# Kernel optimization log

Measured on AMD Instinct MI355X. Metric: run time of the kernel, lower is better.

## Reference

```python
import jax, jax.numpy as jnp
import numpy as np

EPS = 1e-8  # F.cosine_similarity default eps


def setup_inputs() -> dict:
    key = jax.random.key(0)
    k1, k2, k3, k4 = jax.random.split(key, 4)
    N, M, D, BERT_DIM = 8192, 8192, 128, 768
    return {
        "vision_feature": jax.random.normal(k1, (N, D), dtype=jnp.float32),
        "text_pooled": jax.random.normal(k2, (M, BERT_DIM), dtype=jnp.float32),
        "proj_w": jax.random.normal(k3, (D, BERT_DIM), dtype=jnp.float32) * 0.02,
        "proj_b": jax.random.normal(k4, (D,), dtype=jnp.float32) * 0.02,
    }


def reference(vision_feature, text_pooled, proj_w, proj_b):
    # proj(text_pooled): [M, 768] @ [768, D] + [D] -> [M, D]
    text_feature = text_pooled @ proj_w.T + proj_b
    # Fused cosine similarity: L2-normalize rows (with eps clamp as in
    # F.cosine_similarity), then a single [N,D]x[D,M] GEMM instead of the
    # broadcasted O(N*M*D) intermediate.
    v_norm = jnp.maximum(jnp.linalg.norm(vision_feature, axis=1, keepdims=True), EPS)
    t_norm = jnp.maximum(jnp.linalg.norm(text_feature, axis=1, keepdims=True), EPS)
    vn = vision_feature / v_norm  # [N, D]
    tn = text_feature / t_norm    # [M, D]
    similarity = vn @ tn.T        # [N, M]
    return similarity
```

## Files before the change

kernel.cpp:

```cpp
#include <hip/hip_runtime.h>
#include <stdint.h>

#define NV 8192
#define MT 8192
#define DD 128
#define KB 768

typedef __attribute__((ext_vector_type(8))) short short8;
typedef __attribute__((ext_vector_type(4))) float f32x4;

__device__ __forceinline__ ushort f2bf(float f) {
  uint32_t u = __float_as_uint(f);
  u += 0x7FFF + ((u >> 16) & 1);
  return (ushort)(u >> 16);
}

__global__ __launch_bounds__(256) void k_visnorm(const float* __restrict__ vis,
                                                 ushort* __restrict__ vn) {
  const int tx = threadIdx.x & 15;
  const int r  = blockIdx.x * 16 + (threadIdx.x >> 4);
  const float* p = vis + (size_t)r * DD + tx * 8;
  float4 a = *(const float4*)p;
  float4 b = *(const float4*)(p + 4);
  float s = a.x*a.x + a.y*a.y + a.z*a.z + a.w*a.w
          + b.x*b.x + b.y*b.y + b.z*b.z + b.w*b.w;
  s += __shfl_xor(s, 1, 16);
  s += __shfl_xor(s, 2, 16);
  s += __shfl_xor(s, 4, 16);
  s += __shfl_xor(s, 8, 16);
  const float inv = 1.0f / fmaxf(sqrtf(s), 1e-8f);
  union { ushort u[8]; uint4 v; } o;
  o.u[0] = f2bf(a.x * inv); o.u[1] = f2bf(a.y * inv);
  o.u[2] = f2bf(a.z * inv); o.u[3] = f2bf(a.w * inv);
  o.u[4] = f2bf(b.x * inv); o.u[5] = f2bf(b.y * inv);
  o.u[6] = f2bf(b.z * inv); o.u[7] = f2bf(b.w * inv);
  *(uint4*)(vn + (size_t)r * DD + tx * 8) = o.v;
}

__global__ __launch_bounds__(256) void k_cvt(const float* __restrict__ src,
                                             ushort* __restrict__ dst) {
  const size_t i = ((size_t)blockIdx.x * 256 + threadIdx.x) * 8;
  float4 a = *(const float4*)(src + i);
  float4 b = *(const float4*)(src + i + 4);
  union { ushort u[8]; uint4 v; } o;
  o.u[0] = f2bf(a.x); o.u[1] = f2bf(a.y); o.u[2] = f2bf(a.z); o.u[3] = f2bf(a.w);
  o.u[4] = f2bf(b.x); o.u[5] = f2bf(b.y); o.u[6] = f2bf(b.z); o.u[7] = f2bf(b.w);
  *(uint4*)(dst + i) = o.v;
}

__global__ __launch_bounds__(64) void k_projnorm(const ushort* __restrict__ tb,
                                                 const ushort* __restrict__ wb,
                                                 const float* __restrict__ bias,
                                                 ushort* __restrict__ tn) {
  const int lane = threadIdx.x;
  const int row0 = blockIdx.x * 16;
  const int lrow = lane & 15;
  const int g    = lane >> 4;
  const int koff = g * 8;

  const ushort* ap = tb + (size_t)(row0 + lrow) * KB + koff;
  const ushort* bp = wb + (size_t)lrow * KB + koff;

  f32x4 acc[8] = {};

#pragma unroll 4
  for (int ks = 0; ks < KB / 32; ++ks) {
    short8 a = *(const short8*)(ap + ks * 32);
#pragma unroll
    for (int n = 0; n < 8; ++n) {
      short8 b = *(const short8*)(bp + (size_t)n * 16 * KB + ks * 32);
      acc[n] = __builtin_amdgcn_mfma_f32_16x16x32_bf16(a, b, acc[n], 0, 0, 0);
    }
  }

#pragma unroll
  for (int n = 0; n < 8; ++n) {
    float bv = bias[n * 16 + lrow];
#pragma unroll
    for (int j = 0; j < 4; ++j) acc[n][j] += bv;
  }
  float s0 = 0.f, s1 = 0.f, s2 = 0.f, s3 = 0.f;
#pragma unroll
  for (int n = 0; n < 8; ++n) {
    s0 += acc[n][0] * acc[n][0];
    s1 += acc[n][1] * acc[n][1];
    s2 += acc[n][2] * acc[n][2];
    s3 += acc[n][3] * acc[n][3];
  }
#pragma unroll
  for (int d = 1; d < 16; d <<= 1) {
    s0 += __shfl_xor(s0, d, 16);
    s1 += __shfl_xor(s1, d, 16);
    s2 += __shfl_xor(s2, d, 16);
    s3 += __shfl_xor(s3, d, 16);
  }
  float inv[4];
  inv[0] = 1.0f / fmaxf(sqrtf(s0), 1e-8f);
  inv[1] = 1.0f / fmaxf(sqrtf(s1), 1e-8f);
  inv[2] = 1.0f / fmaxf(sqrtf(s2), 1e-8f);
  inv[3] = 1.0f / fmaxf(sqrtf(s3), 1e-8f);

#pragma unroll
  for (int n = 0; n < 8; ++n)
#pragma unroll
    for (int j = 0; j < 4; ++j)
      tn[(size_t)(row0 + g * 4 + j) * DD + n * 16 + lrow] = f2bf(acc[n][j] * inv[j]);
}

__global__ __launch_bounds__(256, 2) void k_sim(const ushort* __restrict__ vn,
                                                const ushort* __restrict__ tn,
                                                float* __restrict__ out) {
  __shared__ ushort ls[32768];
  ushort* lsA = ls;
  ushort* lsB = ls + 16384;
  float*  lsf = (float*)ls;

  const int lin  = blockIdx.x;
  const int nlin = (lin & 7) * 512 + (lin >> 3);
  const int by   = nlin >> 6;
  const int bx   = nlin & 63;
  const int row0 = by * 128;
  const int col0 = bx * 128;

  const int t    = threadIdx.x;
  const int lane = t & 63;
  const int wave = t >> 6;

#pragma unroll
  for (int i = 0; i < 8; ++i) {
    const int fi  = i * 256 + t;
    const int row = fi >> 4;
    uint4 va = *(const uint4*)(vn + (size_t)row0 * DD + fi * 8);
    uint4 vb = *(const uint4*)(tn + (size_t)col0 * DD + fi * 8);
    const int idx = (fi * 8) ^ ((row & 7) << 3);
    *(uint4*)(lsA + idx) = va;
    *(uint4*)(lsB + idx) = vb;
  }
  __syncthreads();

  const int wr = wave >> 1;
  const int wc = wave & 1;
  const int lrow = lane & 15;
  const int kgrp = lane >> 4;

  f32x4 acc[4][4] = {};

#pragma unroll
  for (int ks = 0; ks < 4; ++ks) {
    short8 a[4], b[4];
#pragma unroll
    for (int m = 0; m < 4; ++m) {
      const int r = wr * 64 + m * 16 + lrow;
      const int c = ks * 32 + kgrp * 8;
      a[m] = *(const short8*)(lsA + ((r * 128 + c) ^ ((r & 7) << 3)));
    }
#pragma unroll
    for (int n = 0; n < 4; ++n) {
      const int r = wc * 64 + n * 16 + lrow;
      const int c = ks * 32 + kgrp * 8;
      b[n] = *(const short8*)(lsB + ((r * 128 + c) ^ ((r & 7) << 3)));
    }
#pragma unroll
    for (int m = 0; m < 4; ++m)
#pragma unroll
      for (int n = 0; n < 4; ++n)
        acc[m][n] = __builtin_amdgcn_mfma_f32_16x16x32_bf16(a[m], b[n], acc[m][n], 0, 0, 0);
  }
  __syncthreads();

  const int orow = kgrp * 4;
#pragma unroll
  for (int m = 0; m < 4; ++m)
#pragma unroll
    for (int n = 0; n < 4; ++n) {
      const int r = wr * 64 + m * 16 + orow;
      const int c = wc * 64 + n * 16 + lrow;
#pragma unroll
      for (int j = 0; j < 4; ++j) {
        const int rr = r + j;
        lsf[(rr * 128 + c) ^ (((rr >> 2) & 1) << 4)] = acc[m][n][j];
      }
    }
  __syncthreads();

  const int cr = t >> 5;
  const int cc = (t & 31) * 4;
#pragma unroll
  for (int p = 0; p < 16; ++p) {
    const int r = p * 8 + cr;
    const int idx = (r * 128 + cc) ^ (((r >> 2) & 1) << 4);
    float4 v = *(const float4*)&lsf[idx];
    *(float4*)(out + (size_t)(row0 + r) * MT + col0 + cc) = v;
  }
}

extern "C" void kernel_launch(void* const* d_in, const int* in_sizes, int n_in,
                              void* d_out, int out_size, void* d_ws, size_t ws_size,
                              hipStream_t stream) {
  (void)in_sizes; (void)n_in; (void)out_size; (void)ws_size;
  const float* vis  = (const float*)d_in[0];
  const float* txt  = (const float*)d_in[1];
  const float* w    = (const float*)d_in[2];
  const float* bias = (const float*)d_in[3];
  float* out = (float*)d_out;

  char* ws = (char*)d_ws;
  ushort* vn = (ushort*)(ws);
  ushort* tn = (ushort*)(ws + (size_t)2097152);
  ushort* tb = (ushort*)(ws + (size_t)4194304);
  ushort* wb = (ushort*)(ws + (size_t)16777216);

  k_visnorm<<<NV / 16, 256, 0, stream>>>(vis, vn);
  k_cvt<<<(MT * KB) / 2048, 256, 0, stream>>>(txt, tb);
  k_cvt<<<(DD * KB) / 2048, 256, 0, stream>>>(w, wb);
  k_projnorm<<<MT / 16, 64, 0, stream>>>(tb, wb, bias, tn);
  k_sim<<<4096, 256, 0, stream>>>(vn, tn, out);
}
```

Measured before the change: 124.3 us.

## Fuse text bf16 conversion into projection; enlarge sim tiles with direct global operand loads

Removes the separate fp32->bf16 conversion pass over the 8192x768 text matrix; the projection kernel now reads fp32 text and converts in registers. The similarity kernel moves to 256x256 output tiles with 512 threads. It loads MFMA operands straight from global/L2 instead of staging them through LDS, and writes the output in two LDS-staged halves with nontemporal stores. Both changes aim to cut intermediate traffic, launches and store-side cache pollution. The cost is more register pressure (a 4x8 accumulator array per wave) and uncoalesced global operand loads.

Result: slower. 140.8 us (+13.2%).

```diff
diff --git a/kernel.cpp b/kernel.cpp
--- a/kernel.cpp
+++ b/kernel.cpp
@@ -48,7 +48,7 @@
   *(uint4*)(dst + i) = o.v;
 }
 
-__global__ __launch_bounds__(64) void k_projnorm(const ushort* __restrict__ tb,
+__global__ __launch_bounds__(64) void k_projnorm(const float* __restrict__ txt,
                                                  const ushort* __restrict__ wb,
                                                  const float* __restrict__ bias,
                                                  ushort* __restrict__ tn) {
@@ -58,14 +58,20 @@
   const int g    = lane >> 4;
   const int koff = g * 8;
 
-  const ushort* ap = tb + (size_t)(row0 + lrow) * KB + koff;
+  const float*  ap = txt + (size_t)(row0 + lrow) * KB + koff;
   const ushort* bp = wb + (size_t)lrow * KB + koff;
 
   f32x4 acc[8] = {};
 
 #pragma unroll 4
   for (int ks = 0; ks < KB / 32; ++ks) {
-    short8 a = *(const short8*)(ap + ks * 32);
+    float4 f0 = *(const float4*)(ap + ks * 32);
+    float4 f1 = *(const float4*)(ap + ks * 32 + 4);
+    short8 a;
+    a[0] = (short)f2bf(f0.x); a[1] = (short)f2bf(f0.y);
+    a[2] = (short)f2bf(f0.z); a[3] = (short)f2bf(f0.w);
+    a[4] = (short)f2bf(f1.x); a[5] = (short)f2bf(f1.y);
+    a[6] = (short)f2bf(f1.z); a[7] = (short)f2bf(f1.w);
 #pragma unroll
     for (int n = 0; n < 8; ++n) {
       short8 b = *(const short8*)(bp + (size_t)n * 16 * KB + ks * 32);
@@ -107,90 +113,75 @@
       tn[(size_t)(row0 + g * 4 + j) * DD + n * 16 + lrow] = f2bf(acc[n][j] * inv[j]);
 }
 
-__global__ __launch_bounds__(256, 2) void k_sim(const ushort* __restrict__ vn,
+__global__ __launch_bounds__(512, 2) void k_sim(const ushort* __restrict__ vn,
                                                 const ushort* __restrict__ tn,
                                                 float* __restrict__ out) {
-  __shared__ ushort ls[32768];
-  ushort* lsA = ls;
-  ushort* lsB = ls + 16384;
-  float*  lsf = (float*)ls;
+  __shared__ float lsf[128 * 256];
 
   const int lin  = blockIdx.x;
-  const int nlin = (lin & 7) * 512 + (lin >> 3);
-  const int by   = nlin >> 6;
-  const int bx   = nlin & 63;
-  const int row0 = by * 128;
-  const int col0 = bx * 128;
+  const int nlin = (lin & 7) * 128 + (lin >> 3);
+  const int by   = nlin >> 5;
+  const int bx   = nlin & 31;
+  const int row0 = by * 256;
+  const int col0 = bx * 256;
 
   const int t    = threadIdx.x;
   const int lane = t & 63;
   const int wave = t >> 6;
-
-#pragma unroll
-  for (int i = 0; i < 8; ++i) {
-    const int fi  = i * 256 + t;
-    const int row = fi >> 4;
-    uint4 va = *(const uint4*)(vn + (size_t)row0 * DD + fi * 8);
-    uint4 vb = *(const uint4*)(tn + (size_t)col0 * DD + fi * 8);
-    const int idx = (fi * 8) ^ ((row & 7) << 3);
-    *(uint4*)(lsA + idx) = va;
-    *(uint4*)(lsB + idx) = vb;
-  }
-  __syncthreads();
-
-  const int wr = wave >> 1;
-  const int wc = wave & 1;
+  const int wr   = wave >> 1;
+  const int wc   = wave & 1;
   const int lrow = lane & 15;
   const int kgrp = lane >> 4;
 
-  f32x4 acc[4][4] = {};
+  const ushort* ap = vn + (size_t)(row0 + wr * 64 + lrow) * DD + kgrp * 8;
+  const ushort* bp = tn + (size_t)(col0 + wc * 128 + lrow) * DD + kgrp * 8;
+
+  f32x4 acc[4][8] = {};
 
 #pragma unroll
   for (int ks = 0; ks < 4; ++ks) {
-    short8 a[4], b[4];
-#pragma unroll
-    for (int m = 0; m < 4; ++m) {
-      const int r = wr * 64 + m * 16 + lrow;
-      const int c = ks * 32 + kgrp * 8;
-      a[m] = *(const short8*)(lsA + ((r * 128 + c) ^ ((r & 7) << 3)));
+    short8 a[4], b[8];
+#pragma unroll
+    for (int m = 0; m < 4; ++m)
+      a[m] = *(const short8*)(ap + (size_t)m * 16 * DD + ks * 32);
+#pragma unroll
+    for (int n = 0; n < 8; ++n)
+      b[n] = *(const short8*)(bp + (size_t)n * 16 * DD + ks * 32);
+#pragma unroll
+    for (int m = 0; m < 4; ++m)
+#pragma unroll
+      for (int n = 0; n < 8; ++n)
+        acc[m][n] = __builtin_amdgcn_mfma_f32_16x16x32_bf16(a[m], b[n], acc[m][n], 0, 0, 0);
+  }
+
+#pragma unroll
+  for (int h = 0; h < 2; ++h) {
+    __syncthreads();
+    if ((wr >> 1) == h) {
+      const int rbase = (wr & 1) * 64;
+#pragma unroll
+      for (int m = 0; m < 4; ++m)
+#pragma unroll
+        for (int n = 0; n < 8; ++n) {
+          const int c = wc * 128 + n * 16 + lrow;
+#pragma unroll
+          for (int j = 0; j < 4; ++j) {
+            const int rl = rbase + m * 16 + kgrp * 4 + j;
+            lsf[rl * 256 + (c ^ (((rl >> 2) & 1) << 4))] = acc[m][n][j];
+          }
+        }
     }
-#pragma unroll
-    for (int n = 0; n < 4; ++n) {
-      const int r = wc * 64 + n * 16 + lrow;
-      const int c = ks * 32 + kgrp * 8;
-      b[n] = *(const short8*)(lsB + ((r * 128 + c) ^ ((r & 7) << 3)));
+    __syncthreads();
+    const f32x4* lsf4 = (const f32x4*)lsf;
+#pragma unroll
+    for (int p = 0; p < 16; ++p) {
+      const int fi = p * 512 + t;
+      const int rl = fi >> 6;
+      const int c4 = fi & 63;
+      f32x4 v = lsf4[rl * 64 + (c4 ^ (((rl >> 2) & 1) << 2))];
+      __builtin_nontemporal_store(
+          v, (f32x4*)(out + (size_t)(row0 + h * 128 + rl) * MT + col0 + c4 * 4));
     }
-#pragma unroll
-    for (int m = 0; m < 4; ++m)
-#pragma unroll
-      for (int n = 0; n < 4; ++n)
-        acc[m][n] = __builtin_amdgcn_mfma_f32_16x16x32_bf16(a[m], b[n], acc[m][n], 0, 0, 0);
-  }
-  __syncthreads();
-
-  const int orow = kgrp * 4;
-#pragma unroll
-  for (int m = 0; m < 4; ++m)
-#pragma unroll
-    for (int n = 0; n < 4; ++n) {
-      const int r = wr * 64 + m * 16 + orow;
-      const int c = wc * 64 + n * 16 + lrow;
-#pragma unroll
-      for (int j = 0; j < 4; ++j) {
-        const int rr = r + j;
-        lsf[(rr * 128 + c) ^ (((rr >> 2) & 1) << 4)] = acc[m][n][j];
-      }
-    }
-  __syncthreads();
-
-  const int cr = t >> 5;
-  const int cc = (t & 31) * 4;
-#pragma unroll
-  for (int p = 0; p < 16; ++p) {
-    const int r = p * 8 + cr;
-    const int idx = (r * 128 + cc) ^ (((r >> 2) & 1) << 4);
-    float4 v = *(const float4*)&lsf[idx];
-    *(float4*)(out + (size_t)(row0 + r) * MT + col0 + cc) = v;
   }
 }
 
@@ -207,12 +198,10 @@
   char* ws = (char*)d_ws;
   ushort* vn = (ushort*)(ws);
   ushort* tn = (ushort*)(ws + (size_t)2097152);
-  ushort* tb = (ushort*)(ws + (size_t)4194304);
-  ushort* wb = (ushort*)(ws + (size_t)16777216);
+  ushort* wb = (ushort*)(ws + (size_t)4194304);
 
   k_visnorm<<<NV / 16, 256, 0, stream>>>(vis, vn);
-  k_cvt<<<(MT * KB) / 2048, 256, 0, stream>>>(txt, tb);
   k_cvt<<<(DD * KB) / 2048, 256, 0, stream>>>(w, wb);
-  k_projnorm<<<MT / 16, 64, 0, stream>>>(tb, wb, bias, tn);
-  k_sim<<<4096, 256, 0, stream>>>(vn, tn, out);
-}
+  k_projnorm<<<MT / 16, 64, 0, stream>>>(txt, wb, bias, tn);
+  k_sim<<<1024, 512, 0, stream>>>(vn, tn, out);
+}
```
